# Kernel optimization log

Measured on AMD Instinct MI355X. Metric: run time of the kernel, lower is better.

## Reference

```python
import jax, jax.numpy as jnp
import numpy as np

EPS = 1e-08

def _compute_W(V, C, eps=EPS):
    # W = H_k ... H_1, applied sequentially as in the torch loop
    W = jnp.eye(C, dtype=V.dtype)
    def step(W, v):
        v = v / (jnp.linalg.norm(v) + eps)
        # H @ W = W - 2 v (v^T W)
        W = W - 2.0 * jnp.outer(v, v @ W)
        return W, None
    W, _ = jax.lax.scan(step, W, V)
    return W

def setup_inputs() -> dict:
    key = jax.random.key(0)
    k1, k2 = jax.random.split(key)
    x = jax.random.normal(k1, (16, 512, 64, 64), dtype=jnp.float32)
    V = jax.random.normal(k2, (32, 512), dtype=jnp.float32)
    return {"x": x, "V": V}

def reference(x, V):
    B, C, H, Wd = x.shape
    W = _compute_W(V, C)  # [C, C] orthogonal
    # 1x1 conv: out[b,o,h,w] = sum_c W[o,c] * x[b,c,h,w]
    return jnp.einsum('oc,bchw->bohw', W, x)
```

## Files before the change

### kernel.cpp

```cpp
#include <hip/hip_runtime.h>
#include <hip/hip_bf16.h>
#include <stdint.h>
#include <stddef.h>

#define HH_EPS 1e-8f

typedef __attribute__((ext_vector_type(8))) short short8;
typedef __attribute__((ext_vector_type(4))) short short4_t;
typedef __attribute__((ext_vector_type(4))) float f32x4;

#define CDIM 512
#define SDIM 4096
#define BN 64
#define BK 32
#define NSTEP 16

__device__ __forceinline__ size_t wt_idx(int o, int c) {
    return (((size_t)(c >> 5) * 32 + (o >> 4)) * 64
            + (size_t)((c >> 3) & 3) * 16 + (o & 15)) * 8 + (c & 7);
}

__global__ void compute_w(const float* __restrict__ V,
                          __hip_bfloat16* __restrict__ Wt) {
    const int wave = threadIdx.x >> 6;
    const int lane = threadIdx.x & 63;
    const int jA = (blockIdx.x * 4 + wave) * 2;
    const int jB = jA + 1;
    const int ib = lane * 8;

    float wA[8], wB[8];
    #pragma unroll
    for (int r = 0; r < 8; r++) {
        wA[r] = (ib + r == jA) ? 1.0f : 0.0f;
        wB[r] = (ib + r == jB) ? 1.0f : 0.0f;
    }
    float4 c0 = *(const float4*)(V + ib);
    float4 c1 = *(const float4*)(V + ib + 4);

    for (int k = 0; k < 32; k++) {
        const float v[8] = {c0.x, c0.y, c0.z, c0.w, c1.x, c1.y, c1.z, c1.w};
        if (k < 31) {
            c0 = *(const float4*)(V + (size_t)(k + 1) * 512 + ib);
            c1 = *(const float4*)(V + (size_t)(k + 1) * 512 + ib + 4);
        }
        float dA = 0.0f, dB = 0.0f, ss = 0.0f;
        #pragma unroll
        for (int r = 0; r < 8; r++) {
            dA += v[r] * wA[r];
            dB += v[r] * wB[r];
            ss += v[r] * v[r];
        }
        #pragma unroll
        for (int off = 32; off > 0; off >>= 1) {
            dA += __shfl_xor(dA, off);
            dB += __shfl_xor(dB, off);
            ss += __shfl_xor(ss, off);
        }
        const float t = sqrtf(ss) + HH_EPS;
        const float scale = 2.0f / (t * t);
        const float tA = scale * dA, tB = scale * dB;
        #pragma unroll
        for (int r = 0; r < 8; r++) {
            wA[r] -= tA * v[r];
            wB[r] -= tB * v[r];
        }
    }
    #pragma unroll
    for (int r = 0; r < 8; r++) {
        Wt[wt_idx(ib + r, jA)] = __float2bfloat16(wA[r]);
        Wt[wt_idx(ib + r, jB)] = __float2bfloat16(wB[r]);
    }
}

__device__ __forceinline__ void lds_barrier() {
    __builtin_amdgcn_s_waitcnt(0xC07F);
    __builtin_amdgcn_s_barrier();
}

__global__ __launch_bounds__(512, 4) void hh_gemm(
    const float* __restrict__ x,
    const __hip_bfloat16* __restrict__ Wt,
    float* __restrict__ out)
{
    __shared__ __attribute__((aligned(16))) __hip_bfloat16 Bbuf[2][BN * BK];

    const int tid  = threadIdx.x;
    const int wave = tid >> 6, lane = tid & 63;
    const int quad = lane >> 4, l16 = lane & 15;

    const int bid = blockIdx.x;
    const int b   = bid >> 6;
    const int nt  = bid & 63;
    const int n0  = nt * BN;

    const int bn = tid & 63;
    const int kh = tid >> 6;
    const int kq_s = kh >> 1, h_s = kh & 1;
    const float* xp0 = x + (size_t)b * CDIM * SDIM
                         + (size_t)(kq_s * 8 + h_s * 4) * SDIM + n0 + bn;

    const short8* wp = (const short8*)Wt + (size_t)wave * 4 * 64 + lane;

    f32x4 acc[4][4];
    #pragma unroll
    for (int mi = 0; mi < 4; mi++)
        #pragma unroll
        for (int oi = 0; oi < 4; oi++) {
            f32x4 z = {0.0f, 0.0f, 0.0f, 0.0f};
            acc[mi][oi] = z;
        }

    float  pfB[2][4];
    short8 wb[4];

    auto loadB = [&](int kt, int s) {
        const float* p = xp0 + (size_t)kt * BK * SDIM;
        #pragma unroll
        for (int j = 0; j < 4; j++) pfB[s][j] = p[(size_t)j * SDIM];
    };
    auto writeB = [&](int buf, int s) {
        short4_t pk;
        #pragma unroll
        for (int j = 0; j < 4; j++) {
            __hip_bfloat16 h = __float2bfloat16(pfB[s][j]);
            pk[j] = *(const short*)&h;
        }
        *(short4_t*)(&Bbuf[buf][(size_t)(bn >> 4) * 512
                                + (size_t)(kq_s * 16 + (bn & 15)) * 8
                                + h_s * 4]) = pk;
    };
    auto loadW = [&](int kt) {
        const short8* p = wp + (size_t)kt * 32 * 64;
        #pragma unroll
        for (int oi = 0; oi < 4; oi++) wb[oi] = p[oi * 64];
    };

    loadB(0, 0);
    loadB(1, 1);
    loadW(0);
    writeB(0, 0);
    lds_barrier();

    #pragma unroll
    for (int kt = 0; kt < NSTEP; kt++) {
        if (kt + 2 < NSTEP) loadB(kt + 2, kt & 1);
        const int p = kt & 1;
        #pragma unroll
        for (int mi = 0; mi < 4; mi++) {
            const short8 afr =
                *(const short8*)(&Bbuf[p][(size_t)(mi * 64 + lane) * 8]);
            #pragma unroll
            for (int oi = 0; oi < 4; oi++)
                acc[mi][oi] = __builtin_amdgcn_mfma_f32_16x16x32_bf16(
                    afr, wb[oi], acc[mi][oi], 0, 0, 0);
        }
        if (kt + 1 < NSTEP) {
            loadW(kt + 1);
            writeB(p ^ 1, (kt + 1) & 1);
            lds_barrier();
        }
    }

    float* ob = out + (size_t)b * CDIM * SDIM + n0;
    #pragma unroll
    for (int oi = 0; oi < 4; oi++) {
        const int o = wave * 64 + oi * 16 + l16;
        #pragma unroll
        for (int mi = 0; mi < 4; mi++)
            *(f32x4*)(ob + (size_t)o * SDIM + mi * 16 + quad * 4) = acc[mi][oi];
    }
}

extern "C" void kernel_launch(void* const* d_in, const int* in_sizes, int n_in,
                              void* d_out, int out_size, void* d_ws, size_t ws_size,
                              hipStream_t stream) {
    const float* x = (const float*)d_in[0];
    const float* V = (const float*)d_in[1];
    float* out = (float*)d_out;

    __hip_bfloat16* Wt = (__hip_bfloat16*)d_ws;

    compute_w<<<64, 256, 0, stream>>>(V, Wt);
    hh_gemm<<<1024, 512, 0, stream>>>(x, Wt, out);
}
```

Before: 278.6 us.

## Double spatial tile to 128 with 1024-thread blocks and double-buffer W fragments

Widens the spatial tile from 64 to 128 columns and uses 16 waves per block, each covering 32 output channels across 8 column sub-tiles. This halves the grid to 512 blocks and reuses each W fragment over more columns. W fragments are now double-buffered in registers and prefetched before the MFMA loop instead of after it. In exchange, fewer blocks exist to fill the CUs, and the larger 1024-thread blocks with launch_bounds(1024,4) may limit occupancy or registers.

```diff
diff --git a/kernel.cpp b/kernel.cpp
--- a/kernel.cpp
+++ b/kernel.cpp
@@ -11,7 +11,7 @@
 
 #define CDIM 512
 #define SDIM 4096
-#define BN 64
+#define BN 128
 #define BK 32
 #define NSTEP 16
 
@@ -77,7 +77,7 @@
     __builtin_amdgcn_s_barrier();
 }
 
-__global__ __launch_bounds__(512, 4) void hh_gemm(
+__global__ __launch_bounds__(1024, 4) void hh_gemm(
     const float* __restrict__ x,
     const __hip_bfloat16* __restrict__ Wt,
     float* __restrict__ out)
@@ -89,29 +89,30 @@
     const int quad = lane >> 4, l16 = lane & 15;
 
     const int bid = blockIdx.x;
-    const int b   = bid >> 6;
-    const int nt  = bid & 63;
+    const int b   = bid >> 5;
+    const int nt  = bid & 31;
     const int n0  = nt * BN;
 
-    const int bn = tid & 63;
-    const int kh = tid >> 6;
-    const int kq_s = kh >> 1, h_s = kh & 1;
+    const int c_s  = tid & 127;
+    const int r0_s = (tid >> 7) * 4;
+    const int kq_s = tid >> 8;
+    const int h_s  = (tid >> 7) & 1;
     const float* xp0 = x + (size_t)b * CDIM * SDIM
-                         + (size_t)(kq_s * 8 + h_s * 4) * SDIM + n0 + bn;
+                         + (size_t)r0_s * SDIM + n0 + c_s;
 
-    const short8* wp = (const short8*)Wt + (size_t)wave * 4 * 64 + lane;
+    const short8* wp = (const short8*)Wt + (size_t)(wave * 2) * 64 + lane;
 
-    f32x4 acc[4][4];
+    f32x4 acc[8][2];
     #pragma unroll
-    for (int mi = 0; mi < 4; mi++)
+    for (int mi = 0; mi < 8; mi++)
         #pragma unroll
-        for (int oi = 0; oi < 4; oi++) {
+        for (int oi = 0; oi < 2; oi++) {
             f32x4 z = {0.0f, 0.0f, 0.0f, 0.0f};
             acc[mi][oi] = z;
         }
 
     float  pfB[2][4];
-    short8 wb[4];
+    short8 wb[2][2];
 
     auto loadB = [&](int kt, int s) {
         const float* p = xp0 + (size_t)kt * BK * SDIM;
@@ -125,37 +126,37 @@
             __hip_bfloat16 h = __float2bfloat16(pfB[s][j]);
             pk[j] = *(const short*)&h;
         }
-        *(short4_t*)(&Bbuf[buf][(size_t)(bn >> 4) * 512
-                                + (size_t)(kq_s * 16 + (bn & 15)) * 8
+        *(short4_t*)(&Bbuf[buf][(size_t)(c_s >> 4) * 512
+                                + (size_t)(kq_s * 16 + (c_s & 15)) * 8
                                 + h_s * 4]) = pk;
     };
-    auto loadW = [&](int kt) {
+    auto loadW = [&](int kt, int s) {
         const short8* p = wp + (size_t)kt * 32 * 64;
-        #pragma unroll
-        for (int oi = 0; oi < 4; oi++) wb[oi] = p[oi * 64];
+        wb[s][0] = p[0];
+        wb[s][1] = p[64];
     };
 
     loadB(0, 0);
     loadB(1, 1);
-    loadW(0);
+    loadW(0, 0);
     writeB(0, 0);
     lds_barrier();
 
     #pragma unroll
     for (int kt = 0; kt < NSTEP; kt++) {
+        const int p = kt & 1, w = kt & 1;
+        if (kt + 1 < NSTEP) loadW(kt + 1, w ^ 1);
         if (kt + 2 < NSTEP) loadB(kt + 2, kt & 1);
-        const int p = kt & 1;
         #pragma unroll
-        for (int mi = 0; mi < 4; mi++) {
+        for (int mi = 0; mi < 8; mi++) {
             const short8 afr =
                 *(const short8*)(&Bbuf[p][(size_t)(mi * 64 + lane) * 8]);
             #pragma unroll
-            for (int oi = 0; oi < 4; oi++)
+            for (int oi = 0; oi < 2; oi++)
                 acc[mi][oi] = __builtin_amdgcn_mfma_f32_16x16x32_bf16(
-                    afr, wb[oi], acc[mi][oi], 0, 0, 0);
+                    afr, wb[w][oi], acc[mi][oi], 0, 0, 0);
         }
         if (kt + 1 < NSTEP) {
-            loadW(kt + 1);
             writeB(p ^ 1, (kt + 1) & 1);
             lds_barrier();
         }
@@ -163,10 +164,10 @@
 
     float* ob = out + (size_t)b * CDIM * SDIM + n0;
     #pragma unroll
-    for (int oi = 0; oi < 4; oi++) {
-        const int o = wave * 64 + oi * 16 + l16;
+    for (int oi = 0; oi < 2; oi++) {
+        const int o = wave * 32 + oi * 16 + l16;
         #pragma unroll
-        for (int mi = 0; mi < 4; mi++)
+        for (int mi = 0; mi < 8; mi++)
             *(f32x4*)(ob + (size_t)o * SDIM + mi * 16 + quad * 4) = acc[mi][oi];
     }
 }
@@ -181,5 +182,5 @@
     __hip_bfloat16* Wt = (__hip_bfloat16*)d_ws;
 
     compute_w<<<64, 256, 0, stream>>>(V, Wt);
-    hh_gemm<<<1024, 512, 0, stream>>>(x, Wt, out);
+    hh_gemm<<<512, 1024, 0, stream>>>(x, Wt, out);
 }
```

New measurement: 265.6 us. 4.7% less time.
